# Kernel tuning notes

Hardware: AMD Instinct MI355X
Metric: run time of the kernel (lower is better)

The kernel has to match this reference:

```python
import jax, jax.numpy as jnp
import numpy as np

DIM = 1024
EXPAND = 2
HEAD_DIM = 64
D_STATE = 128
N_GROUPS = 1
D_CONV = 4
D_INNER = DIM * EXPAND            # 2048
N_HEADS = D_INNER // HEAD_DIM     # 32
CONV_DIM = D_INNER + 2 * N_GROUPS * D_STATE  # 2304
D_IN_PROJ = 2 * D_INNER + 2 * N_GROUPS * D_STATE + N_HEADS  # 4384
SEQLEN = 4096
LN_EPS = 1e-5


def setup_inputs() -> dict:
    key = jax.random.key(0)
    ks = jax.random.split(key, 6)
    x = jax.random.normal(ks[0], (SEQLEN, DIM), dtype=jnp.float32)
    W_in = jax.random.normal(ks[1], (D_IN_PROJ, DIM), dtype=jnp.float32) * 0.02
    conv_w = jax.random.normal(ks[2], (CONV_DIM, 1, D_CONV), dtype=jnp.float32) * 0.2
    conv_b = jax.random.normal(ks[3], (CONV_DIM,), dtype=jnp.float32) * 0.02
    # dt_bias init per module: dt ~ exp(U*(log(dt_max)-log(dt_min))+log(dt_min)); inv-softplus
    u = jax.random.uniform(ks[4], (N_HEADS,))
    dt = jnp.exp(u * (np.log(0.1) - np.log(0.001)) + np.log(0.001))
    dt = jnp.clip(dt, 1e-4)
    dt_bias = dt + jnp.log(-jnp.expm1(-dt))
    A_log = jnp.log(jax.random.uniform(ks[5], (N_HEADS,), minval=1.0, maxval=16.0))
    D = jnp.ones((N_HEADS,), dtype=jnp.float32)
    ln_w = jnp.ones((D_INNER,), dtype=jnp.float32)
    ln_b = jnp.zeros((D_INNER,), dtype=jnp.float32)
    W_out = jax.random.normal(jax.random.fold_in(key, 7), (DIM, D_INNER), dtype=jnp.float32) * 0.02
    return {"x": x, "W_in": W_in, "conv_w": conv_w, "conv_b": conv_b,
            "dt_bias": dt_bias, "A_log": A_log, "D": D,
            "ln_w": ln_w, "ln_b": ln_b, "W_out": W_out}


def _forward(x, W_in, conv_w, conv_b, dt_bias, A_log, D, ln_w, ln_b, W_out):
    L = x.shape[0]
    dtype = x.dtype
    A = -jnp.exp(A_log.astype(jnp.float32))  # (h,)
    zxbcdt = x @ W_in.T                       # (L, d_in_proj)
    z = zxbcdt[:, :D_INNER]                   # (L, d_inner)
    xbc = zxbcdt[:, D_INNER:D_INNER + CONV_DIM]
    dt = zxbcdt[:, -N_HEADS:]
    dt = jax.nn.softplus(dt.astype(jnp.float32) + dt_bias.astype(jnp.float32))  # (L, h)
    # depthwise 1D conv, SAME padding (module uses padding='SAME', then slices to L)
    xbc_c = jax.lax.conv_general_dilated(
        xbc.T[None],                          # (1, conv_dim, L)
        conv_w,                               # (conv_dim, 1, k)
        window_strides=(1,), padding='SAME',
        dimension_numbers=('NCH', 'OIH', 'NCH'),
        feature_group_count=CONV_DIM,
    )[0].T + conv_b                           # (L, conv_dim)
    xbc_s = jax.nn.silu(xbc_c)
    x_in = xbc_s[:, :D_INNER].reshape(L, N_HEADS, HEAD_DIM)      # (L, h, p)
    B = xbc_s[:, D_INNER:D_INNER + N_GROUPS * D_STATE]          # (L, n) with g=1
    C = xbc_s[:, D_INNER + N_GROUPS * D_STATE:]                 # (L, n)
    # non-causal linear attention (VSSD): y = C (B^T (x * dt * A)) + x * D
    dA = dt.astype(dtype) * A.astype(dtype)                     # (L, h)
    Vs = x_in * dA[..., None]                                   # (L, h, p)
    KV = jnp.einsum('ln,lhp->hnp', B, Vs)                       # (h, n, p)
    y = jnp.einsum('ln,hnp->lhp', C, KV) + x_in * D[None, :, None]
    y = y.reshape(L, D_INNER)
    # per-token LayerNorm, then multiplicative SiLU(z) gate
    mu = jnp.mean(y, axis=-1, keepdims=True)
    var = jnp.var(y, axis=-1, keepdims=True)
    yn = (y - mu) * jax.lax.rsqrt(var + LN_EPS) * ln_w + ln_b
    y = yn * jax.nn.silu(z)
    return y @ W_out.T                                          # (L, dim)


def reference(x, W_in, conv_w, conv_b, dt_bias, A_log, D, ln_w, ln_b, W_out):
    return _forward(x, W_in, conv_w, conv_b, dt_bias, A_log, D, ln_w, ln_b, W_out)
```

## Files before the change

kernel.cpp:

```cpp
#include <hip/hip_runtime.h>
#include <math.h>

#define SEQLEN    4096
#define DIM_IN    1024
#define D_INNER   2048
#define N_HEADS   32
#define D_STATE   128
#define CONV_DIM  2304
#define D_IN_PROJ 4384
#define PROJ_LD   4480
#define LN_EPS    1e-5f
#define KV_SPLIT  16

typedef __attribute__((ext_vector_type(8))) short bf16x8;
typedef __attribute__((ext_vector_type(4))) float f32x4;
typedef __attribute__((ext_vector_type(8))) short short8;

__device__ __forceinline__ ushort f2bf(float f) {
    union { float f; unsigned u; } v; v.f = f;
    unsigned u = v.u + 0x7FFFu + ((v.u >> 16) & 1u);
    return (ushort)(u >> 16);
}
__device__ __forceinline__ float bf2f(ushort h) {
    union { unsigned u; float f; } v; v.u = ((unsigned)h) << 16;
    return v.f;
}

__device__ __forceinline__ void gload16(const void* g, void* l) {
    __builtin_amdgcn_global_load_lds(
        (const __attribute__((address_space(1))) void*)g,
        (__attribute__((address_space(3))) void*)l, 16, 0, 0);
}

__global__ __launch_bounds__(256)
void cvt_bf16(const float* __restrict__ in, ushort* __restrict__ out, int n8) {
    int i = blockIdx.x * 256 + threadIdx.x;
    if (i >= n8) return;
    float4 v0 = reinterpret_cast<const float4*>(in)[i * 2];
    float4 v1 = reinterpret_cast<const float4*>(in)[i * 2 + 1];
    short8 r;
    r[0] = f2bf(v0.x); r[1] = f2bf(v0.y); r[2] = f2bf(v0.z); r[3] = f2bf(v0.w);
    r[4] = f2bf(v1.x); r[5] = f2bf(v1.y); r[6] = f2bf(v1.z); r[7] = f2bf(v1.w);
    *reinterpret_cast<short8*>(&out[i * 8]) = r;
}

__global__ __launch_bounds__(256)
void cvt_win(const float* __restrict__ in, ushort* __restrict__ out) {
    int i = blockIdx.x * 256 + threadIdx.x;
    const int n8 = PROJ_LD * DIM_IN / 8;
    if (i >= n8) return;
    int row = (i * 8) >> 10;
    short8 r;
    if (row < D_IN_PROJ) {
        float4 v0 = reinterpret_cast<const float4*>(in)[i * 2];
        float4 v1 = reinterpret_cast<const float4*>(in)[i * 2 + 1];
        r[0] = f2bf(v0.x); r[1] = f2bf(v0.y); r[2] = f2bf(v0.z); r[3] = f2bf(v0.w);
        r[4] = f2bf(v1.x); r[5] = f2bf(v1.y); r[6] = f2bf(v1.z); r[7] = f2bf(v1.w);
    } else {
        r = (short8){0,0,0,0,0,0,0,0};
    }
    *reinterpret_cast<short8*>(&out[i * 8]) = r;
}

template<int NT>
__global__ __launch_bounds__(256, 2)
void gemm_bf16_big(const ushort* __restrict__ A, int lda,
                   const ushort* __restrict__ B, int ldb,
                   ushort* __restrict__ Cout, int ldc) {
    __shared__ __align__(16) ushort S[3][12288];

    const int nwg = gridDim.x;
    const int wg  = blockIdx.x;
    const int swz = (wg & 7) * (nwg >> 3) + (wg >> 3);
    const int m0 = (swz & 15) * 256;
    const int n0 = (swz >> 4) * 128;

    const int tid  = threadIdx.x;
    const int wave = tid >> 6;
    const int lane = tid & 63;
    const int wm = (wave >> 1) * 128;
    const int wn = (wave & 1) * 64;
    const int r16 = lane & 15;
    const int kg  = lane >> 4;
    const int pkg = kg ^ ((r16 >> 1) & 3);

    f32x4 acc[8][4];
    #pragma unroll
    for (int i = 0; i < 8; ++i)
        #pragma unroll
        for (int j = 0; j < 4; ++j) acc[i][j] = (f32x4){0.f, 0.f, 0.f, 0.f};

    const int srow = lane >> 2;
    const int scol = ((lane & 3) ^ ((lane >> 3) & 3)) * 8;
    const ushort* gsrc[6];
    #pragma unroll
    for (int i = 0; i < 6; ++i) {
        int c = wave * 6 + i;
        gsrc[i] = (c < 16)
            ? A + (size_t)(m0 + c * 16 + srow) * lda + scol
            : B + (size_t)(n0 + (c - 16) * 16 + srow) * ldb + scol;
    }

#define STAGE_BIG(T, BUF)                                            \
    {                                                                \
        const int _k = (T) * 32;                                     \
        _Pragma("unroll")                                            \
        for (int i = 0; i < 6; ++i)                                  \
            gload16(gsrc[i] + _k, &S[BUF][(wave * 6 + i) * 512]);    \
    }

    STAGE_BIG(0, 0)
    STAGE_BIG(1, 1)

    int rb = 0;
    for (int t = 0; t < NT; ++t) {
        __builtin_amdgcn_sched_barrier(0);
        if (t + 1 < NT) {
            asm volatile("s_waitcnt vmcnt(6)" ::: "memory");
        } else {
            asm volatile("s_waitcnt vmcnt(0)" ::: "memory");
        }
        __builtin_amdgcn_s_barrier();
        __builtin_amdgcn_sched_barrier(0);

        if (t + 2 < NT) {
            int sb = rb + 2; if (sb >= 3) sb -= 3;
            STAGE_BIG(t + 2, sb)
        }

        const ushort* sp = &S[rb][0];
        bf16x8 b4[4];
        #pragma unroll
        for (int ni = 0; ni < 4; ++ni)
            b4[ni] = *reinterpret_cast<const bf16x8*>(
                &sp[8192 + (wn + ni * 16 + r16) * 32 + pkg * 8]);
        #pragma unroll
        for (int mh = 0; mh < 2; ++mh) {
            bf16x8 a4[4];
            #pragma unroll
            for (int i = 0; i < 4; ++i)
                a4[i] = *reinterpret_cast<const bf16x8*>(
                    &sp[(wm + (mh * 4 + i) * 16 + r16) * 32 + pkg * 8]);
            __builtin_amdgcn_s_setprio(1);
            #pragma unroll
            for (int i = 0; i < 4; ++i)
                #pragma unroll
                for (int ni = 0; ni < 4; ++ni)
                    acc[mh * 4 + i][ni] = __builtin_amdgcn_mfma_f32_16x16x32_bf16(
                        a4[i], b4[ni], acc[mh * 4 + i][ni], 0, 0, 0);
            __builtin_amdgcn_s_setprio(0);
        }
        rb = (rb == 2) ? 0 : rb + 1;
    }
#undef STAGE_BIG

    ushort* EP = &S[0][0];
    __syncthreads();
    #pragma unroll
    for (int half = 0; half < 2; ++half) {
        if ((wave >> 1) == half) {
            #pragma unroll
            for (int mi = 0; mi < 8; ++mi)
                #pragma unroll
                for (int ni = 0; ni < 4; ++ni)
                    #pragma unroll
                    for (int r = 0; r < 4; ++r)
                        EP[(mi * 16 + kg * 4 + r) * 136 + wn + ni * 16 + r16] =
                            f2bf(acc[mi][ni][r]);
        }
        __syncthreads();
        #pragma unroll
        for (int i = 0; i < 8; ++i) {
            int idx = tid + 256 * i;
            int row = idx >> 4;
            int cb  = idx & 15;
            bf16x8 v = *reinterpret_cast<const bf16x8*>(&EP[row * 136 + cb * 8]);
            *reinterpret_cast<bf16x8*>(
                &Cout[(size_t)(m0 + half * 128 + row) * ldc + n0 + cb * 8]) = v;
        }
        __syncthreads();
    }
}

template<int BN, int NT, int OUTBF>
__global__ __launch_bounds__(256)
void gemm_bf16_pipe(const ushort* __restrict__ A, int lda,
                    const ushort* __restrict__ B, int ldb,
                    void* __restrict__ Cout, int ldc) {
    constexpr int NI  = BN / 32;
    constexpr int BNP = BN + 8;
    __shared__ __align__(16) ushort As[3][128 * 32];
    __shared__ __align__(16) ushort Bs[3][BN * 32];

    const int nwg = gridDim.x;
    const int wg  = blockIdx.x;
    const int swz = (wg & 7) * (nwg >> 3) + (wg >> 3);
    const int m0 = (swz & 31) * 128;
    const int n0 = (swz >> 5) * BN;

    const int tid  = threadIdx.x;
    const int wave = tid >> 6;
    const int lane = tid & 63;
    const int wm = (wave & 1) * 64;
    const int wn = (wave >> 1) * (BN / 2);
    const int r16 = lane & 15;
    const int kg  = lane >> 4;
    const int pkg = kg ^ ((r16 >> 1) & 3);

    f32x4 acc[4][NI];
    #pragma unroll
    for (int i = 0; i < 4; ++i)
        #pragma unroll
        for (int j = 0; j < NI; ++j) acc[i][j] = (f32x4){0.f, 0.f, 0.f, 0.f};

    const int srow = lane >> 2;
    const int scol = ((lane & 3) ^ ((lane >> 3) & 3)) * 8;
    const int ca0 = wave * 2, ca1 = wave * 2 + 1;
    const ushort* gA0 = A + (size_t)(m0 + ca0 * 16 + srow) * lda + scol;
    const ushort* gA1 = A + (size_t)(m0 + ca1 * 16 + srow) * lda + scol;
    const ushort* gB0;
    const ushort* gB1 = nullptr;
    int cb0, cb1 = 0;
    if constexpr (BN == 128) {
        cb0 = wave * 2; cb1 = wave * 2 + 1;
        gB0 = B + (size_t)(n0 + cb0 * 16 + srow) * ldb + scol;
        gB1 = B + (size_t)(n0 + cb1 * 16 + srow) * ldb + scol;
    } else {
        cb0 = wave;
        gB0 = B + (size_t)(n0 + cb0 * 16 + srow) * ldb + scol;
    }

#define STAGE_STEP(T, BUF)                                          \
    {                                                               \
        const int _k = (T) * 32;                                    \
        gload16(gA0 + _k, &As[BUF][ca0 * 512]);                     \
        gload16(gA1 + _k, &As[BUF][ca1 * 512]);                     \
        gload16(gB0 + _k, &Bs[BUF][cb0 * 512]);                     \
        if constexpr (BN == 128) gload16(gB1 + _k, &Bs[BUF][cb1 * 512]); \
    }

    STAGE_STEP(0, 0)
    STAGE_STEP(1, 1)

    int rb = 0;
    for (int t = 0; t < NT; ++t) {
        __builtin_amdgcn_sched_barrier(0);
        if (t + 1 < NT) {
            if constexpr (BN == 128) asm volatile("s_waitcnt vmcnt(4)" ::: "memory");
            else                     asm volatile("s_waitcnt vmcnt(3)" ::: "memory");
        } else {
            asm volatile("s_waitcnt vmcnt(0)" ::: "memory");
        }
        __builtin_amdgcn_s_barrier();
        __builtin_amdgcn_sched_barrier(0);

        if (t + 2 < NT) {
            int sb = rb + 2; if (sb >= 3) sb -= 3;
            STAGE_STEP(t + 2, sb)
        }

        const ushort* ab = &As[rb][0];
        const ushort* bb = &Bs[rb][0];
        bf16x8 a[4], b[NI];
        #pragma unroll
        for (int mi = 0; mi < 4; ++mi)
            a[mi] = *reinterpret_cast<const bf16x8*>(&ab[(wm + mi * 16 + r16) * 32 + pkg * 8]);
        #pragma unroll
        for (int ni = 0; ni < NI; ++ni)
            b[ni] = *reinterpret_cast<const bf16x8*>(&bb[(wn + ni * 16 + r16) * 32 + pkg * 8]);

        __builtin_amdgcn_s_setprio(1);
        #pragma unroll
        for (int mi = 0; mi < 4; ++mi)
            #pragma unroll
            for (int ni = 0; ni < NI; ++ni)
                acc[mi][ni] = __builtin_amdgcn_mfma_f32_16x16x32_bf16(a[mi], b[ni], acc[mi][ni], 0, 0, 0);
        __builtin_amdgcn_s_setprio(0);

        rb = (rb == 2) ? 0 : rb + 1;
    }
#undef STAGE_STEP

    if constexpr (OUTBF) {
        ushort* EP = &As[0][0];
        ushort* outp = (ushort*)Cout;
        __syncthreads();
        #pragma unroll
        for (int half = 0; half < 2; ++half) {
            if ((wave & 1) == half) {
                #pragma unroll
                for (int mi = 0; mi < 4; ++mi)
                    #pragma unroll
                    for (int ni = 0; ni < NI; ++ni)
                        #pragma unroll
                        for (int r = 0; r < 4; ++r)
                            EP[(mi * 16 + kg * 4 + r) * BNP + wn + ni * 16 + r16] =
                                f2bf(acc[mi][ni][r]);
            }
            __syncthreads();
            #pragma unroll
            for (int i = 0; i < BN / 32; ++i) {
                int idx = tid + 256 * i;
                int row = idx / (BN / 8);
                int cb  = idx % (BN / 8);
                bf16x8 v = *reinterpret_cast<const bf16x8*>(&EP[row * BNP + cb * 8]);
                *reinterpret_cast<bf16x8*>(
                    &outp[(size_t)(m0 + half * 64 + row) * ldc + n0 + cb * 8]) = v;
            }
            __syncthreads();
        }
    } else {
        float* outp = (float*)Cout;
        #pragma unroll
        for (int mi = 0; mi < 4; ++mi)
            #pragma unroll
            for (int ni = 0; ni < NI; ++ni)
                #pragma unroll
                for (int r = 0; r < 4; ++r) {
                    int row = m0 + wm + mi * 16 + kg * 4 + r;
                    int col = n0 + wn + ni * 16 + r16;
                    outp[(size_t)row * ldc + col] = acc[mi][ni][r];
                }
    }
}

__global__ __launch_bounds__(256)
void conv_silu_kernel(const ushort* __restrict__ zxb,
                      const float* __restrict__ conv_w,
                      const float* __restrict__ conv_b,
                      const float* __restrict__ dt_bias,
                      const float* __restrict__ A_log,
                      ushort* __restrict__ xbcs,
                      float* __restrict__ dA) {
    const int l = blockIdx.x;
    const ushort* base = zxb + (size_t)l * PROJ_LD + D_INNER;
    for (int c = threadIdx.x; c < CONV_DIM; c += 256) {
        float w0 = conv_w[c * 4 + 0], w1 = conv_w[c * 4 + 1];
        float w2 = conv_w[c * 4 + 2], w3 = conv_w[c * 4 + 3];
        float acc = conv_b[c];
        if (l >= 1)          acc += w0 * bf2f(base[c - PROJ_LD]);
        acc += w1 * bf2f(base[c]);
        if (l + 1 < SEQLEN)  acc += w2 * bf2f(base[c + PROJ_LD]);
        if (l + 2 < SEQLEN)  acc += w3 * bf2f(base[c + 2 * PROJ_LD]);
        float s = acc / (1.0f + expf(-acc));
        xbcs[(size_t)l * CONV_DIM + c] = f2bf(s);
    }
    if (threadIdx.x < N_HEADS) {
        int h = threadIdx.x;
        float v = bf2f(zxb[(size_t)l * PROJ_LD + (D_IN_PROJ - N_HEADS) + h]) + dt_bias[h];
        float sp = (v > 20.0f) ? v : log1pf(expf(v));
        dA[l * N_HEADS + h] = sp * (-expf(A_log[h]));
    }
}

__global__ __launch_bounds__(256)
void kv_kernel(const ushort* __restrict__ xbcs,
               const float* __restrict__ dA,
               float* __restrict__ KVp) {
    __shared__ float Vs[16][132];
    __shared__ float Bsm[16][132];
    const int hp0 = blockIdx.x * 128;
    const int lc0 = blockIdx.y * (SEQLEN / KV_SPLIT);
    const int tid = threadIdx.x;
    const int ty = tid >> 4, tx = tid & 15;
    float acc[8][8];
    #pragma unroll
    for (int i = 0; i < 8; ++i)
        #pragma unroll
        for (int j = 0; j < 8; ++j) acc[i][j] = 0.0f;

    for (int ls = 0; ls < SEQLEN / KV_SPLIT; ls += 16) {
        {
            int lrow = tid >> 4;
            int p8   = (tid & 15) * 8;
            int l = lc0 + ls + lrow;
            short8 v = *reinterpret_cast<const short8*>(
                &xbcs[(size_t)l * CONV_DIM + hp0 + p8]);
            float a = dA[l * N_HEADS + ((hp0 + p8) >> 6)];
            #pragma unroll
            for (int j = 0; j < 8; ++j) Vs[lrow][p8 + j] = bf2f((ushort)v[j]) * a;
            short8 b = *reinterpret_cast<const short8*>(
                &xbcs[(size_t)l * CONV_DIM + D_INNER + p8]);
            #pragma unroll
            for (int j = 0; j < 8; ++j) Bsm[lrow][p8 + j] = bf2f((ushort)b[j]);
        }
        __syncthreads();
        #pragma unroll
        for (int k = 0; k < 16; ++k) {
            float a[8], b[8];
            *reinterpret_cast<float4*>(&a[0]) = *reinterpret_cast<const float4*>(&Vs[k][ty * 8]);
            *reinterpret_cast<float4*>(&a[4]) = *reinterpret_cast<const float4*>(&Vs[k][ty * 8 + 4]);
            *reinterpret_cast<float4*>(&b[0]) = *reinterpret_cast<const float4*>(&Bsm[k][tx * 8]);
            *reinterpret_cast<float4*>(&b[4]) = *reinterpret_cast<const float4*>(&Bsm[k][tx * 8 + 4]);
            #pragma unroll
            for (int i = 0; i < 8; ++i)
                #pragma unroll
                for (int j = 0; j < 8; ++j)
                    acc[i][j] = fmaf(a[i], b[j], acc[i][j]);
        }
        __syncthreads();
    }
    float* dst = KVp + (size_t)blockIdx.y * (D_INNER * D_STATE);
    #pragma unroll
    for (int i = 0; i < 8; ++i) {
        int hp = hp0 + ty * 8 + i;
        #pragma unroll
        for (int j = 0; j < 8; j += 4) {
            float4 v = make_float4(acc[i][j], acc[i][j+1], acc[i][j+2], acc[i][j+3]);
            *reinterpret_cast<float4*>(&dst[(size_t)hp * D_STATE + tx * 8 + j]) = v;
        }
    }
}

__global__ __launch_bounds__(256)
void kv_reduce(const float* __restrict__ KVp, ushort* __restrict__ KVTb) {
    int i = blockIdx.x * 256 + threadIdx.x;
    float4 s = make_float4(0.f, 0.f, 0.f, 0.f);
    #pragma unroll
    for (int c = 0; c < KV_SPLIT; ++c) {
        float4 v = reinterpret_cast<const float4*>(KVp + (size_t)c * (D_INNER * D_STATE))[i];
        s.x += v.x; s.y += v.y; s.z += v.z; s.w += v.w;
    }
    ushort4 o;
    o.x = f2bf(s.x); o.y = f2bf(s.y); o.z = f2bf(s.z); o.w = f2bf(s.w);
    *reinterpret_cast<ushort4*>(&KVTb[i * 4]) = o;
}

__global__ __launch_bounds__(256)
void ln_gate_kernel(const ushort* __restrict__ y1b,
                    const ushort* __restrict__ xbcs,
                    const ushort* __restrict__ zxb,
                    const float* __restrict__ Dp,
                    const float* __restrict__ ln_w,
                    const float* __restrict__ ln_b,
                    ushort* __restrict__ yb) {
    const int l = blockIdx.x;
    const int tid = threadIdx.x;
    const int c = tid * 8;
    float y[8], z[8];
    float sum = 0.f, sumsq = 0.f;
    {
        short8 v  = *reinterpret_cast<const short8*>(&y1b[(size_t)l * D_INNER + c]);
        short8 xi = *reinterpret_cast<const short8*>(&xbcs[(size_t)l * CONV_DIM + c]);
        short8 zz = *reinterpret_cast<const short8*>(&zxb[(size_t)l * PROJ_LD + c]);
        float d = Dp[c >> 6];
        #pragma unroll
        for (int j = 0; j < 8; ++j) {
            float yv = bf2f((ushort)v[j]) + bf2f((ushort)xi[j]) * d;
            y[j] = yv;
            z[j] = bf2f((ushort)zz[j]);
            sum += yv;
            sumsq += yv * yv;
        }
    }
    #pragma unroll
    for (int off = 32; off > 0; off >>= 1) {
        sum   += __shfl_down(sum, off);
        sumsq += __shfl_down(sumsq, off);
    }
    __shared__ float red[8];
    int wid = tid >> 6;
    if ((tid & 63) == 0) { red[wid] = sum; red[4 + wid] = sumsq; }
    __syncthreads();
    sum   = red[0] + red[1] + red[2] + red[3];
    sumsq = red[4] + red[5] + red[6] + red[7];
    float mu  = sum * (1.0f / D_INNER);
    float var = sumsq * (1.0f / D_INNER) - mu * mu;
    float rs  = rsqrtf(var + LN_EPS);
    short8 o;
    #pragma unroll
    for (int j = 0; j < 8; ++j) {
        float yn = (y[j] - mu) * rs * ln_w[c + j] + ln_b[c + j];
        float g  = z[j] / (1.0f + expf(-z[j]));
        o[j] = f2bf(yn * g);
    }
    *reinterpret_cast<short8*>(&yb[(size_t)l * D_INNER + c]) = o;
}

extern "C" void kernel_launch(void* const* d_in, const int* in_sizes, int n_in,
                              void* d_out, int out_size, void* d_ws, size_t ws_size,
                              hipStream_t stream) {
    const float* x       = (const float*)d_in[0];
    const float* W_in    = (const float*)d_in[1];
    const float* conv_w  = (const float*)d_in[2];
    const float* conv_b  = (const float*)d_in[3];
    const float* dt_bias = (const float*)d_in[4];
    const float* A_log   = (const float*)d_in[5];
    const float* Dp      = (const float*)d_in[6];
    const float* ln_w    = (const float*)d_in[7];
    const float* ln_b    = (const float*)d_in[8];
    const float* W_out   = (const float*)d_in[9];
    float* out = (float*)d_out;

    char* ws = (char*)d_ws;
    ushort* zxb   = (ushort*)ws;
    ushort* xbcs  = (ushort*)(ws +  36700160);
    ushort* y1b   = (ushort*)(ws +  55574528);
    ushort* yb    = (ushort*)(ws +  72351744);
    float*  KVp   = (float*)(ws +  89128960);
    float*  dA    = (float*)(ws + 105906176);
    ushort* KVTb  = (ushort*)(ws + 106430464);
    ushort* Woutb = (ushort*)(ws + 106954752);
    ushort* xb    = (ushort*)(ws + 111149056);
    ushort* Winb  = (ushort*)(ws + 119537664);

    cvt_bf16<<<(SEQLEN * DIM_IN / 8 + 255) / 256, 256, 0, stream>>>(x, xb, SEQLEN * DIM_IN / 8);
    cvt_win<<<(PROJ_LD * DIM_IN / 8 + 255) / 256, 256, 0, stream>>>(W_in, Winb);
    cvt_bf16<<<(DIM_IN * D_INNER / 8 + 255) / 256, 256, 0, stream>>>(W_out, Woutb, DIM_IN * D_INNER / 8);

    gemm_bf16_big<32><<<16 * (PROJ_LD / 128), 256, 0, stream>>>(
        xb, DIM_IN, Winb, DIM_IN, zxb, PROJ_LD);

    conv_silu_kernel<<<SEQLEN, 256, 0, stream>>>(zxb, conv_w, conv_b, dt_bias, A_log,
                                                 xbcs, dA);

    kv_kernel<<<dim3(16, KV_SPLIT), 256, 0, stream>>>(xbcs, dA, KVp);
    kv_reduce<<<(D_INNER * D_STATE / 4) / 256, 256, 0, stream>>>(KVp, KVTb);

    gemm_bf16_pipe<128, 4, 1><<<(D_INNER / 128) * 32, 256, 0, stream>>>(
        xbcs + (D_INNER + D_STATE), CONV_DIM, KVTb, D_STATE, y1b, D_INNER);

    ln_gate_kernel<<<SEQLEN, 256, 0, stream>>>(y1b, xbcs, zxb, Dp, ln_w, ln_b, yb);

    gemm_bf16_pipe<64, 64, 0><<<(DIM_IN / 64) * 32, 256, 0, stream>>>(
        yb, D_INNER, Woutb, D_INNER, out, DIM_IN);
}
```

Before: 208.2 us.

## Merge conversion kernels, vectorize conv-SiLU, and reorder GEMM tile mapping

Combines the three fp32-to-bf16 conversion launches into a single kernel indexed over all three buffers, which removes two launches. The depthwise conv+SiLU kernel now processes 8 channels per thread using 16-byte vector loads and stores instead of scalar accesses. The GEMM tile index mapping changes from M-major to N-fastest through a new template parameter, which alters which blocks share A/B tiles in cache. The cost is extra divergence in the merged conversion kernel and a changed L2 reuse pattern.

New measurement: 199.4 us. -4.2%, faster.

```diff
diff --git a/kernel.cpp b/kernel.cpp
--- a/kernel.cpp
+++ b/kernel.cpp
@@ -32,37 +32,42 @@
         (__attribute__((address_space(3))) void*)l, 16, 0, 0);
 }
 
+#define XB_GROUPS   (SEQLEN * DIM_IN / 8)
+#define WIN_GROUPS  (PROJ_LD * DIM_IN / 8)
+#define WOUT_GROUPS (DIM_IN * D_INNER / 8)
 __global__ __launch_bounds__(256)
-void cvt_bf16(const float* __restrict__ in, ushort* __restrict__ out, int n8) {
+void cvt_all(const float* __restrict__ x, const float* __restrict__ W_in,
+             const float* __restrict__ W_out,
+             ushort* __restrict__ xb, ushort* __restrict__ Winb,
+             ushort* __restrict__ Woutb) {
     int i = blockIdx.x * 256 + threadIdx.x;
-    if (i >= n8) return;
-    float4 v0 = reinterpret_cast<const float4*>(in)[i * 2];
-    float4 v1 = reinterpret_cast<const float4*>(in)[i * 2 + 1];
+    const float* src;
+    ushort* dst;
+    int gi;
+    if (i < XB_GROUPS) {
+        src = x; dst = xb; gi = i;
+    } else if (i < XB_GROUPS + WIN_GROUPS) {
+        gi = i - XB_GROUPS;
+        int row = (gi * 8) >> 10;
+        if (row >= D_IN_PROJ) {
+            *reinterpret_cast<short8*>(&Winb[(size_t)gi * 8]) = (short8){0,0,0,0,0,0,0,0};
+            return;
+        }
+        src = W_in; dst = Winb;
+    } else if (i < XB_GROUPS + WIN_GROUPS + WOUT_GROUPS) {
+        gi = i - (XB_GROUPS + WIN_GROUPS);
+        src = W_out; dst = Woutb;
+    } else return;
+    float4 v0 = reinterpret_cast<const float4*>(src)[gi * 2];
+    float4 v1 = reinterpret_cast<const float4*>(src)[gi * 2 + 1];
     short8 r;
     r[0] = f2bf(v0.x); r[1] = f2bf(v0.y); r[2] = f2bf(v0.z); r[3] = f2bf(v0.w);
     r[4] = f2bf(v1.x); r[5] = f2bf(v1.y); r[6] = f2bf(v1.z); r[7] = f2bf(v1.w);
-    *reinterpret_cast<short8*>(&out[i * 8]) = r;
-}
-
-__global__ __launch_bounds__(256)
-void cvt_win(const float* __restrict__ in, ushort* __restrict__ out) {
-    int i = blockIdx.x * 256 + threadIdx.x;
-    const int n8 = PROJ_LD * DIM_IN / 8;
-    if (i >= n8) return;
-    int row = (i * 8) >> 10;
-    short8 r;
-    if (row < D_IN_PROJ) {
-        float4 v0 = reinterpret_cast<const float4*>(in)[i * 2];
-        float4 v1 = reinterpret_cast<const float4*>(in)[i * 2 + 1];
-        r[0] = f2bf(v0.x); r[1] = f2bf(v0.y); r[2] = f2bf(v0.z); r[3] = f2bf(v0.w);
-        r[4] = f2bf(v1.x); r[5] = f2bf(v1.y); r[6] = f2bf(v1.z); r[7] = f2bf(v1.w);
-    } else {
-        r = (short8){0,0,0,0,0,0,0,0};
-    }
-    *reinterpret_cast<short8*>(&out[i * 8]) = r;
-}
-
-template<int NT>
+    *reinterpret_cast<short8*>(&dst[(size_t)gi * 8]) = r;
+}
+#define CVT_TOTAL (XB_GROUPS + WIN_GROUPS + WOUT_GROUPS)
+
+template<int NT, int NTB>
 __global__ __launch_bounds__(256, 2)
 void gemm_bf16_big(const ushort* __restrict__ A, int lda,
                    const ushort* __restrict__ B, int ldb,
@@ -72,8 +77,8 @@
     const int nwg = gridDim.x;
     const int wg  = blockIdx.x;
     const int swz = (wg & 7) * (nwg >> 3) + (wg >> 3);
-    const int m0 = (swz & 15) * 256;
-    const int n0 = (swz >> 4) * 128;
+    const int m0 = (swz / NTB) * 256;
+    const int n0 = (swz % NTB) * 128;
 
     const int tid  = threadIdx.x;
     const int wave = tid >> 6;
@@ -182,7 +187,7 @@
     }
 }
 
-template<int BN, int NT, int OUTBF>
+template<int BN, int NT, int OUTBF, int NTB>
 __global__ __launch_bounds__(256)
 void gemm_bf16_pipe(const ushort* __restrict__ A, int lda,
                     const ushort* __restrict__ B, int ldb,
@@ -195,8 +200,8 @@
     const int nwg = gridDim.x;
     const int wg  = blockIdx.x;
     const int swz = (wg & 7) * (nwg >> 3) + (wg >> 3);
-    const int m0 = (swz & 31) * 128;
-    const int n0 = (swz >> 5) * BN;
+    const int m0 = (swz / NTB) * 128;
+    const int n0 = (swz % NTB) * BN;
 
     const int tid  = threadIdx.x;
     const int wave = tid >> 6;
@@ -334,16 +339,33 @@
                       float* __restrict__ dA) {
     const int l = blockIdx.x;
     const ushort* base = zxb + (size_t)l * PROJ_LD + D_INNER;
-    for (int c = threadIdx.x; c < CONV_DIM; c += 256) {
-        float w0 = conv_w[c * 4 + 0], w1 = conv_w[c * 4 + 1];
-        float w2 = conv_w[c * 4 + 2], w3 = conv_w[c * 4 + 3];
-        float acc = conv_b[c];
-        if (l >= 1)          acc += w0 * bf2f(base[c - PROJ_LD]);
-        acc += w1 * bf2f(base[c]);
-        if (l + 1 < SEQLEN)  acc += w2 * bf2f(base[c + PROJ_LD]);
-        if (l + 2 < SEQLEN)  acc += w3 * bf2f(base[c + 2 * PROJ_LD]);
-        float s = acc / (1.0f + expf(-acc));
-        xbcs[(size_t)l * CONV_DIM + c] = f2bf(s);
+    const short8 zero8 = (short8){0,0,0,0,0,0,0,0};
+    for (int g = threadIdx.x; g < CONV_DIM / 8; g += 256) {
+        const int c = g * 8;
+        short8 xm = (l >= 1)
+            ? *reinterpret_cast<const short8*>(base + c - PROJ_LD) : zero8;
+        short8 x0 = *reinterpret_cast<const short8*>(base + c);
+        short8 xp = (l + 1 < SEQLEN)
+            ? *reinterpret_cast<const short8*>(base + c + PROJ_LD) : zero8;
+        short8 xq = (l + 2 < SEQLEN)
+            ? *reinterpret_cast<const short8*>(base + c + 2 * PROJ_LD) : zero8;
+        float4 bia0 = *reinterpret_cast<const float4*>(&conv_b[c]);
+        float4 bia1 = *reinterpret_cast<const float4*>(&conv_b[c + 4]);
+        const float* bp = &bia0.x;
+        short8 o;
+        #pragma unroll
+        for (int j = 0; j < 8; ++j) {
+            float4 w = *reinterpret_cast<const float4*>(&conv_w[(c + j) * 4]);
+            float acc = (j < 4 ? (&bia0.x)[j] : (&bia1.x)[j - 4]);
+            acc += w.x * bf2f((ushort)xm[j]);
+            acc += w.y * bf2f((ushort)x0[j]);
+            acc += w.z * bf2f((ushort)xp[j]);
+            acc += w.w * bf2f((ushort)xq[j]);
+            float s = acc / (1.0f + expf(-acc));
+            o[j] = f2bf(s);
+        }
+        (void)bp;
+        *reinterpret_cast<short8*>(&xbcs[(size_t)l * CONV_DIM + c]) = o;
     }
     if (threadIdx.x < N_HEADS) {
         int h = threadIdx.x;
@@ -504,11 +526,9 @@
     ushort* xb    = (ushort*)(ws + 111149056);
     ushort* Winb  = (ushort*)(ws + 119537664);
 
-    cvt_bf16<<<(SEQLEN * DIM_IN / 8 + 255) / 256, 256, 0, stream>>>(x, xb, SEQLEN * DIM_IN / 8);
-    cvt_win<<<(PROJ_LD * DIM_IN / 8 + 255) / 256, 256, 0, stream>>>(W_in, Winb);
-    cvt_bf16<<<(DIM_IN * D_INNER / 8 + 255) / 256, 256, 0, stream>>>(W_out, Woutb, DIM_IN * D_INNER / 8);
-
-    gemm_bf16_big<32><<<16 * (PROJ_LD / 128), 256, 0, stream>>>(
+    cvt_all<<<(CVT_TOTAL + 255) / 256, 256, 0, stream>>>(x, W_in, W_out, xb, Winb, Woutb);
+
+    gemm_bf16_big<32, 35><<<16 * (PROJ_LD / 128), 256, 0, stream>>>(
         xb, DIM_IN, Winb, DIM_IN, zxb, PROJ_LD);
 
     conv_silu_kernel<<<SEQLEN, 256, 0, stream>>>(zxb, conv_w, conv_b, dt_bias, A_log,
@@ -517,11 +537,11 @@
     kv_kernel<<<dim3(16, KV_SPLIT), 256, 0, stream>>>(xbcs, dA, KVp);
     kv_reduce<<<(D_INNER * D_STATE / 4) / 256, 256, 0, stream>>>(KVp, KVTb);
 
-    gemm_bf16_pipe<128, 4, 1><<<(D_INNER / 128) * 32, 256, 0, stream>>>(
+    gemm_bf16_pipe<128, 4, 1, 16><<<(D_INNER / 128) * 32, 256, 0, stream>>>(
         xbcs + (D_INNER + D_STATE), CONV_DIM, KVTb, D_STATE, y1b, D_INNER);
 
     ln_gate_kernel<<<SEQLEN, 256, 0, stream>>>(y1b, xbcs, zxb, Dp, ln_w, ln_b, yb);
 
-    gemm_bf16_pipe<64, 64, 0><<<(DIM_IN / 64) * 32, 256, 0, stream>>>(
+    gemm_bf16_pipe<64, 64, 0, 16><<<(DIM_IN / 64) * 32, 256, 0, stream>>>(
         yb, D_INNER, Woutb, D_INNER, out, DIM_IN);
 }
```
